# Optimization experiments

Measured on AMD Instinct MI355X. Metric: run time of the kernel, lower is better.

Reference implementation:

```python
import jax, jax.numpy as jnp
import numpy as np

N_NODES = 50000
N_HEDGES = 25000
E_NN = 800000
E_HH = 400000
E_INC = 200000
D = 128


def setup_inputs() -> dict:
    key = jax.random.key(0)
    ks = jax.random.split(key, 24)
    s = 1.0 / np.sqrt(D)
    inp = {
        'node_features': jax.random.normal(ks[0], (N_NODES, D), jnp.float32),
        'hedge_features': jax.random.normal(ks[1], (N_HEDGES, D), jnp.float32),
        'W_node_msg': jax.random.normal(ks[2], (D, D), jnp.float32) * s,
        'b_node_msg': jax.random.normal(ks[3], (D,), jnp.float32) * s,
        'W_hedge_scale': jax.random.normal(ks[4], (D, D), jnp.float32) * s,
        'b_hedge_scale': jax.random.normal(ks[5], (D,), jnp.float32) * s,
        'W_hedge_msg': jax.random.normal(ks[6], (D, D), jnp.float32) * s,
        'b_hedge_msg': jax.random.normal(ks[7], (D,), jnp.float32) * s,
        'W_node_scale': jax.random.normal(ks[8], (D, D), jnp.float32) * s,
        'b_node_scale': jax.random.normal(ks[9], (D,), jnp.float32) * s,
        'node_convolution': jax.random.uniform(ks[10], (E_NN, 1), jnp.float32),
        'hedge2node_convolution': jax.random.uniform(ks[11], (E_INC, 1), jnp.float32),
        'hedge_convolution': jax.random.uniform(ks[12], (E_HH, 1), jnp.float32),
        'node2hedge_convolution': jax.random.uniform(ks[13], (E_INC, 1), jnp.float32),
        'node_senders': jax.random.randint(ks[14], (E_NN,), 0, N_NODES, jnp.int32),
        'node_receivers': jax.random.randint(ks[15], (E_NN,), 0, N_NODES, jnp.int32),
        'hedge2node_senders': jax.random.randint(ks[16], (E_INC,), 0, N_HEDGES, jnp.int32),
        'hedge2node_receivers': jax.random.randint(ks[17], (E_INC,), 0, N_NODES, jnp.int32),
        'hedge_senders': jax.random.randint(ks[18], (E_HH,), 0, N_HEDGES, jnp.int32),
        'hedge_receivers': jax.random.randint(ks[19], (E_HH,), 0, N_HEDGES, jnp.int32),
        'node2hedge_senders': jax.random.randint(ks[20], (E_INC,), 0, N_NODES, jnp.int32),
        'node2hedge_receivers': jax.random.randint(ks[21], (E_INC,), 0, N_HEDGES, jnp.int32),
    }
    return inp


def _lin(x, W, b):
    # eqx.nn.Linear: y = W @ x + b, vmapped over rows -> x @ W.T + b
    return x @ W.T + b


def reference(node_features, hedge_features,
              W_node_msg, b_node_msg, W_hedge_scale, b_hedge_scale,
              W_hedge_msg, b_hedge_msg, W_node_scale, b_node_scale,
              node_convolution, hedge2node_convolution,
              hedge_convolution, node2hedge_convolution,
              node_senders, node_receivers,
              hedge2node_senders, hedge2node_receivers,
              hedge_senders, hedge_receivers,
              node2hedge_senders, node2hedge_receivers):
    n_nodes = node_features.shape[0]
    n_hedges = hedge_features.shape[0]

    # --- NodeConvolution ---
    msgs = _lin(node_features[node_senders], W_node_msg, b_node_msg)  # [E_nn, D]
    gathered_msgs = jax.ops.segment_sum(node_convolution * msgs, node_receivers,
                                        num_segments=n_nodes)
    h_msgs = _lin(hedge_features[hedge2node_senders], W_hedge_scale, b_hedge_scale)
    gathered_scale = jax.ops.segment_sum(hedge2node_convolution * h_msgs,
                                         hedge2node_receivers, num_segments=n_nodes)
    new_node_features = jnp.tanh(gathered_scale * gathered_msgs)

    # --- HedgeConvolution (uses updated node features) ---
    e_msgs = _lin(hedge_features[hedge_senders], W_hedge_msg, b_hedge_msg)  # [E_hh, D]
    gathered_e = jax.ops.segment_sum(hedge_convolution * e_msgs, hedge_receivers,
                                     num_segments=n_hedges)
    n_msgs = _lin(new_node_features[node2hedge_senders], W_node_scale, b_node_scale)
    gathered_n = jax.ops.segment_sum(node2hedge_convolution * n_msgs,
                                     node2hedge_receivers, num_segments=n_hedges)
    new_hedge_features = jnp.tanh(gathered_n * gathered_e)

    return (new_node_features, new_hedge_features)
```

## Files before the change

kernel.cpp:

```cpp
#include <hip/hip_runtime.h>
#include <hip/hip_bf16.h>

#define N_NODES  50000
#define N_HEDGES 25000
#define E_NN     800000
#define E_HH     400000
#define E_INC    200000
#define D        128

__global__ __launch_bounds__(256) void swizzleW(
    const float* __restrict__ w0, const float* __restrict__ w1,
    const float* __restrict__ w2, const float* __restrict__ w3,
    float* __restrict__ out) {
  int id = blockIdx.x * 256 + threadIdx.x;
  int m = id >> 14, r = id & 16383;
  const float* w = (m == 0) ? w0 : (m == 1) ? w1 : (m == 2) ? w2 : w3;
  int c = r >> 7, k = r & 127;
  out[m * 16512 + (c >> 2) * 516 + (k >> 2) * 16 + (c & 3) * 4 + (k & 3)] = w[r];
}

__global__ __launch_bounds__(256) void linear64(
    const float* __restrict__ X, const float* __restrict__ Wz,
    const float* __restrict__ bias, float* __restrict__ Y, int n) {
  __shared__ float Ws[16 * 516];
  __shared__ float Xs[64 * 132];
  int t = threadIdx.x;
  int r0 = blockIdx.x * 64;
  int cb = blockIdx.y * 64;

  const float* wsrc = Wz + blockIdx.y * (16 * 516);
  for (int i = t * 4; i < 16 * 516; i += 1024)
    *(float4*)(Ws + i) = *(const float4*)(wsrc + i);

  for (int q = t; q < 2048; q += 256) {
    int r = q >> 5, k4 = q & 31;
    float4 v = (r0 + r < n) ? *(const float4*)(X + (size_t)(r0 + r) * D + k4 * 4)
                            : make_float4(0.f, 0.f, 0.f, 0.f);
    *(float4*)(&Xs[r * 132 + k4 * 4]) = v;
  }
  __syncthreads();

  int tr = t >> 4, tc = t & 15;
  float acc[4][4] = {};
  const float* xbase = &Xs[tr * 4 * 132];
  const float* wbase = &Ws[tc * 516];

#pragma unroll 8
  for (int k4 = 0; k4 < 32; ++k4) {
    float4 xv[4], wv[4];
#pragma unroll
    for (int i = 0; i < 4; ++i) xv[i] = *(const float4*)(xbase + i * 132 + k4 * 4);
#pragma unroll
    for (int j = 0; j < 4; ++j) wv[j] = *(const float4*)(wbase + k4 * 16 + j * 4);
#pragma unroll
    for (int i = 0; i < 4; ++i)
#pragma unroll
      for (int j = 0; j < 4; ++j)
        acc[i][j] += xv[i].x * wv[j].x + xv[i].y * wv[j].y +
                     xv[i].z * wv[j].z + xv[i].w * wv[j].w;
  }

  int c0 = cb + tc * 4;
  float4 bv = *(const float4*)(bias + c0);
#pragma unroll
  for (int i = 0; i < 4; ++i) {
    int r = r0 + tr * 4 + i;
    if (r < n) {
      float4 o;
      o.x = acc[i][0] + bv.x; o.y = acc[i][1] + bv.y;
      o.z = acc[i][2] + bv.z; o.w = acc[i][3] + bv.w;
      *(float4*)(Y + (size_t)r * D + c0) = o;
    }
  }
}

#define B_NN   3125
#define B_H2N  782
#define B_HH   1563
#define B_N2H  782
#define B_TOT  (B_NN + B_H2N + B_HH + B_N2H)

__global__ __launch_bounds__(256) void hist4(
    const int* __restrict__ rNN, const int* __restrict__ rH2N,
    const int* __restrict__ rHH, const int* __restrict__ rN2H,
    int* __restrict__ cNN, int* __restrict__ cH2N,
    int* __restrict__ cHH, int* __restrict__ cN2H) {
  int b = blockIdx.x;
  const int* rcv; int* cnt; int E, base;
  if (b < B_NN)                { rcv = rNN;  cnt = cNN;  E = E_NN;  base = 0; }
  else if (b < B_NN + B_H2N)   { rcv = rH2N; cnt = cH2N; E = E_INC; base = B_NN; }
  else if (b < B_NN + B_H2N + B_HH) { rcv = rHH; cnt = cHH; E = E_HH; base = B_NN + B_H2N; }
  else                         { rcv = rN2H; cnt = cN2H; E = E_INC; base = B_NN + B_H2N + B_HH; }
  int i = (b - base) * 256 + threadIdx.x;
  if (i < E) atomicAdd(&cnt[rcv[i]], 1);
}

__global__ __launch_bounds__(1024) void exscan4(
    const int* __restrict__ c0, int* __restrict__ o0, int* __restrict__ u0,
    const int* __restrict__ c1, int* __restrict__ o1, int* __restrict__ u1,
    const int* __restrict__ c2, int* __restrict__ o2, int* __restrict__ u2,
    const int* __restrict__ c3, int* __restrict__ o3, int* __restrict__ u3) {
  const int* c; int* offs; int* cur; int n;
  switch (blockIdx.x) {
    case 0:  c = c0; offs = o0; cur = u0; n = N_NODES;  break;
    case 1:  c = c1; offs = o1; cur = u1; n = N_NODES;  break;
    case 2:  c = c2; offs = o2; cur = u2; n = N_HEDGES; break;
    default: c = c3; offs = o3; cur = u3; n = N_HEDGES; break;
  }
  __shared__ int wsum[16];
  __shared__ int carrySh;
  int lane = threadIdx.x & 63, wid = threadIdx.x >> 6;
  if (threadIdx.x == 0) carrySh = 0;
  __syncthreads();
  for (int base = 0; base < n; base += 4096) {
    int i0 = base + threadIdx.x * 4;
    int v[4];
#pragma unroll
    for (int j = 0; j < 4; ++j) { int i = i0 + j; v[j] = (i < n) ? c[i] : 0; }
    int s = v[0] + v[1] + v[2] + v[3];
    int inc = s;
#pragma unroll
    for (int off = 1; off < 64; off <<= 1) {
      int tv = __shfl_up(inc, off, 64);
      if (lane >= off) inc += tv;
    }
    if (lane == 63) wsum[wid] = inc;
    __syncthreads();
    if (threadIdx.x == 0) {
      int run = 0;
      for (int w = 0; w < 16; ++w) { int x = wsum[w]; wsum[w] = run; run += x; }
    }
    __syncthreads();
    int run = carrySh + wsum[wid] + (inc - s);
#pragma unroll
    for (int j = 0; j < 4; ++j) {
      int i = i0 + j;
      if (i < n) { offs[i] = run; cur[i] = run; }
      run += v[j];
    }
    __syncthreads();
    if (threadIdx.x == 1023) carrySh = run;
    __syncthreads();
  }
  if (threadIdx.x == 0) offs[n] = carrySh;
}

__global__ __launch_bounds__(256) void fill4(
    const int* __restrict__ rNN, const int* __restrict__ sNN,
    const float* __restrict__ vNN, int* __restrict__ uNN, int2* __restrict__ pNN,
    const int* __restrict__ rH2N, const int* __restrict__ sH2N,
    const float* __restrict__ vH2N, int* __restrict__ uH2N, int2* __restrict__ pH2N,
    const int* __restrict__ rHH, const int* __restrict__ sHH,
    const float* __restrict__ vHH, int* __restrict__ uHH, int2* __restrict__ pHH,
    const int* __restrict__ rN2H, const int* __restrict__ sN2H,
    const float* __restrict__ vN2H, int* __restrict__ uN2H, int2* __restrict__ pN2H) {
  int b = blockIdx.x;
  const int* rcv; const int* snd; const float* cv; int* cur; int2* pr; int E, base;
  if (b < B_NN)                { rcv = rNN;  snd = sNN;  cv = vNN;  cur = uNN;  pr = pNN;  E = E_NN;  base = 0; }
  else if (b < B_NN + B_H2N)   { rcv = rH2N; snd = sH2N; cv = vH2N; cur = uH2N; pr = pH2N; E = E_INC; base = B_NN; }
  else if (b < B_NN + B_H2N + B_HH) { rcv = rHH; snd = sHH; cv = vHH; cur = uHH; pr = pHH; E = E_HH; base = B_NN + B_H2N; }
  else                         { rcv = rN2H; snd = sN2H; cv = vN2H; cur = uN2H; pr = pN2H; E = E_INC; base = B_NN + B_H2N + B_HH; }
  int i = (b - base) * 256 + threadIdx.x;
  if (i < E) {
    int p = atomicAdd(&cur[rcv[i]], 1);
    pr[p] = make_int2(snd[i], __float_as_int(cv[i]));
  }
}

__global__ __launch_bounds__(256) void gather_combine2(
    const float* __restrict__ Pa, const int2* __restrict__ pairsA,
    const int* __restrict__ offsA,
    const float* __restrict__ Pb, const int2* __restrict__ pairsB,
    const int* __restrict__ offsB,
    float* __restrict__ out, int nrows) {
  int row = (blockIdx.x << 2) | (threadIdx.x >> 6);
  if (row >= nrows) return;
  int lane = threadIdx.x & 63;

  float sax = 0.f, say = 0.f;
  {
    int a0 = offsA[row], a1 = offsA[row + 1];
    int i = a0;
    for (; i + 8 <= a1; i += 8) {
      int2 p[8]; float2 v[8];
#pragma unroll
      for (int j = 0; j < 8; ++j) p[j] = pairsA[i + j];
#pragma unroll
      for (int j = 0; j < 8; ++j)
        v[j] = *(const float2*)(Pa + (size_t)p[j].x * D + lane * 2);
#pragma unroll
      for (int j = 0; j < 8; ++j) {
        float c = __int_as_float(p[j].y);
        sax += c * v[j].x; say += c * v[j].y;
      }
    }
    for (; i + 4 <= a1; i += 4) {
      int2 p[4]; float2 v[4];
#pragma unroll
      for (int j = 0; j < 4; ++j) p[j] = pairsA[i + j];
#pragma unroll
      for (int j = 0; j < 4; ++j)
        v[j] = *(const float2*)(Pa + (size_t)p[j].x * D + lane * 2);
#pragma unroll
      for (int j = 0; j < 4; ++j) {
        float c = __int_as_float(p[j].y);
        sax += c * v[j].x; say += c * v[j].y;
      }
    }
    for (; i < a1; ++i) {
      int2 p = pairsA[i];
      float c = __int_as_float(p.y);
      float2 v = *(const float2*)(Pa + (size_t)p.x * D + lane * 2);
      sax += c * v.x; say += c * v.y;
    }
  }

  float sbx = 0.f, sby = 0.f;
  {
    int b0 = offsB[row], b1 = offsB[row + 1];
    int i = b0;
    for (; i + 4 <= b1; i += 4) {
      int2 p[4]; float2 v[4];
#pragma unroll
      for (int j = 0; j < 4; ++j) p[j] = pairsB[i + j];
#pragma unroll
      for (int j = 0; j < 4; ++j)
        v[j] = *(const float2*)(Pb + (size_t)p[j].x * D + lane * 2);
#pragma unroll
      for (int j = 0; j < 4; ++j) {
        float c = __int_as_float(p[j].y);
        sbx += c * v[j].x; sby += c * v[j].y;
      }
    }
    for (; i < b1; ++i) {
      int2 p = pairsB[i];
      float c = __int_as_float(p.y);
      float2 v = *(const float2*)(Pb + (size_t)p.x * D + lane * 2);
      sbx += c * v.x; sby += c * v.y;
    }
  }

  float2 o;
  o.x = tanhf(sax * sbx);
  o.y = tanhf(say * sby);
  *(float2*)(out + (size_t)row * D + lane * 2) = o;
}

extern "C" void kernel_launch(void* const* d_in, const int* in_sizes, int n_in,
                              void* d_out, int out_size, void* d_ws, size_t ws_size,
                              hipStream_t stream) {
  const float* node_features  = (const float*)d_in[0];
  const float* hedge_features = (const float*)d_in[1];
  const float* W_node_msg     = (const float*)d_in[2];
  const float* b_node_msg     = (const float*)d_in[3];
  const float* W_hedge_scale  = (const float*)d_in[4];
  const float* b_hedge_scale  = (const float*)d_in[5];
  const float* W_hedge_msg    = (const float*)d_in[6];
  const float* b_hedge_msg    = (const float*)d_in[7];
  const float* W_node_scale   = (const float*)d_in[8];
  const float* b_node_scale   = (const float*)d_in[9];
  const float* node_conv      = (const float*)d_in[10];
  const float* h2n_conv       = (const float*)d_in[11];
  const float* hedge_conv     = (const float*)d_in[12];
  const float* n2h_conv       = (const float*)d_in[13];
  const int*   node_snd       = (const int*)d_in[14];
  const int*   node_rcv       = (const int*)d_in[15];
  const int*   h2n_snd        = (const int*)d_in[16];
  const int*   h2n_rcv        = (const int*)d_in[17];
  const int*   hedge_snd      = (const int*)d_in[18];
  const int*   hedge_rcv      = (const int*)d_in[19];
  const int*   n2h_snd        = (const int*)d_in[20];
  const int*   n2h_rcv        = (const int*)d_in[21];

  float* out_node  = (float*)d_out;
  float* out_hedge = (float*)d_out + (size_t)N_NODES * D;

  float* ws = (float*)d_ws;
  float* Wz = ws;
  float* PA = ws + 66048;
  float* PB = PA + (size_t)N_NODES * D;
  int2* pairsNN  = (int2*)(PB + (size_t)N_HEDGES * D);
  int2* pairsH2N = pairsNN + E_NN;
  int2* pairsHH  = pairsH2N + E_INC;
  int2* pairsN2H = pairsHH + E_HH;
  int* cntNN  = (int*)(pairsN2H + E_INC);
  int* cntH2N = cntNN + N_NODES;
  int* cntHH  = cntH2N + N_NODES;
  int* cntN2H = cntHH + N_HEDGES;
  int* curNN  = cntN2H + N_HEDGES;
  int* curH2N = curNN + N_NODES;
  int* curHH  = curH2N + N_NODES;
  int* curN2H = curHH + N_HEDGES;
  int* offsNN  = curN2H + N_HEDGES;
  int* offsH2N = offsNN + N_NODES + 1;
  int* offsHH  = offsH2N + N_NODES + 1;
  int* offsN2H = offsHH + N_HEDGES + 1;

  swizzleW<<<256, 256, 0, stream>>>(W_node_msg, W_hedge_scale, W_hedge_msg,
                                    W_node_scale, Wz);
  hipMemsetAsync(cntNN, 0, (size_t)(2 * (N_NODES + N_HEDGES)) * sizeof(int), stream);

  hist4<<<B_TOT, 256, 0, stream>>>(node_rcv, h2n_rcv, hedge_rcv, n2h_rcv,
                                   cntNN, cntH2N, cntHH, cntN2H);
  exscan4<<<4, 1024, 0, stream>>>(cntNN, offsNN, curNN,
                                  cntH2N, offsH2N, curH2N,
                                  cntHH, offsHH, curHH,
                                  cntN2H, offsN2H, curN2H);
  fill4<<<B_TOT, 256, 0, stream>>>(
      node_rcv, node_snd, node_conv, curNN, pairsNN,
      h2n_rcv, h2n_snd, h2n_conv, curH2N, pairsH2N,
      hedge_rcv, hedge_snd, hedge_conv, curHH, pairsHH,
      n2h_rcv, n2h_snd, n2h_conv, curN2H, pairsN2H);

  linear64<<<dim3(782, 2), 256, 0, stream>>>(node_features, Wz + 0 * 16512,
                                             b_node_msg, PA, N_NODES);
  linear64<<<dim3(391, 2), 256, 0, stream>>>(hedge_features, Wz + 1 * 16512,
                                             b_hedge_scale, PB, N_HEDGES);
  gather_combine2<<<N_NODES / 4, 256, 0, stream>>>(
      PA, pairsNN, offsNN, PB, pairsH2N, offsH2N, out_node, N_NODES);

  linear64<<<dim3(391, 2), 256, 0, stream>>>(hedge_features, Wz + 2 * 16512,
                                             b_hedge_msg, PB, N_HEDGES);
  linear64<<<dim3(782, 2), 256, 0, stream>>>(out_node, Wz + 3 * 16512,
                                             b_node_scale, PA, N_NODES);
  gather_combine2<<<N_HEDGES / 4, 256, 0, stream>>>(
      PB, pairsHH, offsHH, PA, pairsN2H, offsN2H, out_hedge, N_HEDGES);
}
```

Before: 602.4 us.

## Replace serial scan and scatter fill with parallel scan and two-pass bucketed CSR build

The single-block-per-array exclusive scan becomes a three-kernel multi-block scan (block scans, scan of block sums, add-back). The one-pass atomic scatter fill becomes a two-pass bucketed scatter. Pass A groups edges into 64-receiver buckets using shared-memory histograms and per-bucket global atomics. Pass B places each bucket's edges into final CSR positions, so the scattered writes stay local. This targets the serial scan latency and the poorly coalesced random scatter, at the cost of extra kernel launches and an intermediate record buffer that is written and read once.

Result: faster. 548.0 us (-9.0%).

```diff
diff --git a/kernel.cpp b/kernel.cpp
--- a/kernel.cpp
+++ b/kernel.cpp
@@ -95,75 +95,187 @@
   if (i < E) atomicAdd(&cnt[rcv[i]], 1);
 }
 
-__global__ __launch_bounds__(1024) void exscan4(
-    const int* __restrict__ c0, int* __restrict__ o0, int* __restrict__ u0,
-    const int* __restrict__ c1, int* __restrict__ o1, int* __restrict__ u1,
-    const int* __restrict__ c2, int* __restrict__ o2, int* __restrict__ u2,
-    const int* __restrict__ c3, int* __restrict__ o3, int* __restrict__ u3) {
-  const int* c; int* offs; int* cur; int n;
-  switch (blockIdx.x) {
-    case 0:  c = c0; offs = o0; cur = u0; n = N_NODES;  break;
-    case 1:  c = c1; offs = o1; cur = u1; n = N_NODES;  break;
-    case 2:  c = c2; offs = o2; cur = u2; n = N_HEDGES; break;
-    default: c = c3; offs = o3; cur = u3; n = N_HEDGES; break;
-  }
-  __shared__ int wsum[16];
-  __shared__ int carrySh;
-  int lane = threadIdx.x & 63, wid = threadIdx.x >> 6;
-  if (threadIdx.x == 0) carrySh = 0;
-  __syncthreads();
-  for (int base = 0; base < n; base += 4096) {
-    int i0 = base + threadIdx.x * 4;
-    int v[4];
-#pragma unroll
-    for (int j = 0; j < 4; ++j) { int i = i0 + j; v[j] = (i < n) ? c[i] : 0; }
-    int s = v[0] + v[1] + v[2] + v[3];
-    int inc = s;
-#pragma unroll
-    for (int off = 1; off < 64; off <<= 1) {
-      int tv = __shfl_up(inc, off, 64);
-      if (lane >= off) inc += tv;
-    }
-    if (lane == 63) wsum[wid] = inc;
-    __syncthreads();
-    if (threadIdx.x == 0) {
-      int run = 0;
-      for (int w = 0; w < 16; ++w) { int x = wsum[w]; wsum[w] = run; run += x; }
-    }
-    __syncthreads();
-    int run = carrySh + wsum[wid] + (inc - s);
-#pragma unroll
-    for (int j = 0; j < 4; ++j) {
-      int i = i0 + j;
-      if (i < n) { offs[i] = run; cur[i] = run; }
-      run += v[j];
-    }
-    __syncthreads();
-    if (threadIdx.x == 1023) carrySh = run;
-    __syncthreads();
-  }
-  if (threadIdx.x == 0) offs[n] = carrySh;
-}
-
-__global__ __launch_bounds__(256) void fill4(
-    const int* __restrict__ rNN, const int* __restrict__ sNN,
-    const float* __restrict__ vNN, int* __restrict__ uNN, int2* __restrict__ pNN,
-    const int* __restrict__ rH2N, const int* __restrict__ sH2N,
-    const float* __restrict__ vH2N, int* __restrict__ uH2N, int2* __restrict__ pH2N,
-    const int* __restrict__ rHH, const int* __restrict__ sHH,
-    const float* __restrict__ vHH, int* __restrict__ uHH, int2* __restrict__ pHH,
-    const int* __restrict__ rN2H, const int* __restrict__ sN2H,
-    const float* __restrict__ vN2H, int* __restrict__ uN2H, int2* __restrict__ pN2H) {
+#define SB_NN0  0
+#define SB_H2N0 25
+#define SB_HH0  50
+#define SB_N2H0 63
+#define SB_TOT  76
+
+__global__ __launch_bounds__(256) void scan_blk(
+    const int* __restrict__ cNN, const int* __restrict__ cH2N,
+    const int* __restrict__ cHH, const int* __restrict__ cN2H,
+    int* __restrict__ oNN, int* __restrict__ oH2N,
+    int* __restrict__ oHH, int* __restrict__ oN2H,
+    int* __restrict__ bsum) {
   int b = blockIdx.x;
-  const int* rcv; const int* snd; const float* cv; int* cur; int2* pr; int E, base;
-  if (b < B_NN)                { rcv = rNN;  snd = sNN;  cv = vNN;  cur = uNN;  pr = pNN;  E = E_NN;  base = 0; }
-  else if (b < B_NN + B_H2N)   { rcv = rH2N; snd = sH2N; cv = vH2N; cur = uH2N; pr = pH2N; E = E_INC; base = B_NN; }
-  else if (b < B_NN + B_H2N + B_HH) { rcv = rHH; snd = sHH; cv = vHH; cur = uHH; pr = pHH; E = E_HH; base = B_NN + B_H2N; }
-  else                         { rcv = rN2H; snd = sN2H; cv = vN2H; cur = uN2H; pr = pN2H; E = E_INC; base = B_NN + B_H2N + B_HH; }
-  int i = (b - base) * 256 + threadIdx.x;
-  if (i < E) {
-    int p = atomicAdd(&cur[rcv[i]], 1);
-    pr[p] = make_int2(snd[i], __float_as_int(cv[i]));
+  const int* c; int* o; int n; int lb;
+  if (b < SB_H2N0)       { c = cNN;  o = oNN;  n = N_NODES;  lb = b; }
+  else if (b < SB_HH0)   { c = cH2N; o = oH2N; n = N_NODES;  lb = b - SB_H2N0; }
+  else if (b < SB_N2H0)  { c = cHH;  o = oHH;  n = N_HEDGES; lb = b - SB_HH0; }
+  else                   { c = cN2H; o = oN2H; n = N_HEDGES; lb = b - SB_N2H0; }
+  int t = threadIdx.x, lane = t & 63, wid = t >> 6;
+  int i0 = lb * 2048 + t * 8;
+  int v[8]; int s = 0;
+#pragma unroll
+  for (int j = 0; j < 8; ++j) { int i = i0 + j; v[j] = (i < n) ? c[i] : 0; s += v[j]; }
+  int inc = s;
+#pragma unroll
+  for (int off = 1; off < 64; off <<= 1) {
+    int tv = __shfl_up(inc, off, 64);
+    if (lane >= off) inc += tv;
+  }
+  __shared__ int wsum[4];
+  if (lane == 63) wsum[wid] = inc;
+  __syncthreads();
+  if (t == 0) {
+    int run = 0;
+    for (int w = 0; w < 4; ++w) { int x = wsum[w]; wsum[w] = run; run += x; }
+  }
+  __syncthreads();
+  int run = wsum[wid] + (inc - s);
+#pragma unroll
+  for (int j = 0; j < 8; ++j) { int i = i0 + j; if (i < n) o[i] = run; run += v[j]; }
+  if (t == 255) bsum[b] = run;
+}
+
+__global__ void scan_bsum(int* __restrict__ bsum,
+                          int* __restrict__ oNN, int* __restrict__ oH2N,
+                          int* __restrict__ oHH, int* __restrict__ oN2H) {
+  int a = threadIdx.x;
+  if (a >= 4) return;
+  int base = (a == 0) ? SB_NN0 : (a == 1) ? SB_H2N0 : (a == 2) ? SB_HH0 : SB_N2H0;
+  int cnt  = (a < 2) ? 25 : 13;
+  int run = 0;
+  for (int i = 0; i < cnt; ++i) { int x = bsum[base + i]; bsum[base + i] = run; run += x; }
+  int* o = (a == 0) ? oNN : (a == 1) ? oH2N : (a == 2) ? oHH : oN2H;
+  int n = (a < 2) ? N_NODES : N_HEDGES;
+  o[n] = run;
+}
+
+__global__ __launch_bounds__(256) void scan_add(
+    int* __restrict__ oNN, int* __restrict__ oH2N,
+    int* __restrict__ oHH, int* __restrict__ oN2H,
+    int* __restrict__ uNN, int* __restrict__ uH2N,
+    int* __restrict__ uHH, int* __restrict__ uN2H,
+    const int* __restrict__ bsum) {
+  int b = blockIdx.x;
+  int* o; int* u; int n; int lb;
+  if (b < SB_H2N0)       { o = oNN;  u = uNN;  n = N_NODES;  lb = b; }
+  else if (b < SB_HH0)   { o = oH2N; u = uH2N; n = N_NODES;  lb = b - SB_H2N0; }
+  else if (b < SB_N2H0)  { o = oHH;  u = uHH;  n = N_HEDGES; lb = b - SB_HH0; }
+  else                   { o = oN2H; u = uN2H; n = N_HEDGES; lb = b - SB_N2H0; }
+  int add = bsum[b];
+  int i0 = lb * 2048 + threadIdx.x * 8;
+#pragma unroll
+  for (int j = 0; j < 8; ++j) {
+    int i = i0 + j;
+    if (i < n) { int x = o[i] + add; o[i] = x; u[i] = x; }
+  }
+}
+
+#define NB_NN   782
+#define NB_H2N  782
+#define NB_HH   391
+#define NB_N2H  391
+#define NB_TOT  (NB_NN + NB_H2N + NB_HH + NB_N2H)
+#define NB_MAX  782
+
+#define REC_NN  0
+#define REC_H2N 800000
+#define REC_HH  1000000
+#define REC_N2H 1400000
+
+__global__ __launch_bounds__(256) void initb(
+    const int* __restrict__ oNN, const int* __restrict__ oH2N,
+    const int* __restrict__ oHH, const int* __restrict__ oN2H,
+    int* __restrict__ bcur) {
+  int i = blockIdx.x * 256 + threadIdx.x;
+  if (i >= NB_TOT) return;
+  int v;
+  if (i < NB_NN)                        v = oNN[i << 6];
+  else if (i < NB_NN + NB_H2N)          v = oH2N[(i - NB_NN) << 6];
+  else if (i < NB_NN + NB_H2N + NB_HH)  v = oHH[(i - NB_NN - NB_H2N) << 6];
+  else                                  v = oN2H[(i - NB_NN - NB_H2N - NB_HH) << 6];
+  bcur[i] = v;
+}
+
+#define PA_NN0  0
+#define PA_H2N0 391
+#define PA_HH0  489
+#define PA_N2H0 685
+#define PA_TOT  783
+
+__global__ __launch_bounds__(256) void passA(
+    const int* __restrict__ sNN, const int* __restrict__ rNN, const float* __restrict__ vNN,
+    const int* __restrict__ sH2N, const int* __restrict__ rH2N, const float* __restrict__ vH2N,
+    const int* __restrict__ sHH, const int* __restrict__ rHH, const float* __restrict__ vHH,
+    const int* __restrict__ sN2H, const int* __restrict__ rN2H, const float* __restrict__ vN2H,
+    int* __restrict__ bcur, int2* __restrict__ rec_sc, int* __restrict__ rec_r) {
+  __shared__ int hist[NB_MAX];
+  __shared__ int gbase[NB_MAX];
+  __shared__ int lcur[NB_MAX];
+  int b = blockIdx.x;
+  const int* snd; const int* rcv; const float* conv;
+  int E, blkbase, bcoff, recoff, NB;
+  if (b < PA_H2N0)      { snd=sNN;  rcv=rNN;  conv=vNN;  E=E_NN;  blkbase=PA_NN0;  bcoff=0;    recoff=REC_NN;  NB=NB_NN; }
+  else if (b < PA_HH0)  { snd=sH2N; rcv=rH2N; conv=vH2N; E=E_INC; blkbase=PA_H2N0; bcoff=782;  recoff=REC_H2N; NB=NB_H2N; }
+  else if (b < PA_N2H0) { snd=sHH;  rcv=rHH;  conv=vHH;  E=E_HH;  blkbase=PA_HH0;  bcoff=1564; recoff=REC_HH;  NB=NB_HH; }
+  else                  { snd=sN2H; rcv=rN2H; conv=vN2H; E=E_INC; blkbase=PA_N2H0; bcoff=1955; recoff=REC_N2H; NB=NB_N2H; }
+  int t = threadIdx.x;
+  int estart = (b - blkbase) * 2048;
+
+  int rv[8]; int sd[8]; float cv[8]; int bk[8]; bool ok[8];
+#pragma unroll
+  for (int j = 0; j < 8; ++j) {
+    int e = estart + t + j * 256;
+    ok[j] = e < E;
+    int r = ok[j] ? rcv[e] : 0;
+    rv[j] = r;
+    bk[j] = r >> 6;
+    sd[j] = ok[j] ? snd[e] : 0;
+    cv[j] = ok[j] ? conv[e] : 0.f;
+  }
+  for (int i = t; i < NB; i += 256) hist[i] = 0;
+  __syncthreads();
+#pragma unroll
+  for (int j = 0; j < 8; ++j) if (ok[j]) atomicAdd(&hist[bk[j]], 1);
+  __syncthreads();
+  for (int i = t; i < NB; i += 256) {
+    int h = hist[i];
+    gbase[i] = h ? atomicAdd(&bcur[bcoff + i], h) : 0;
+    lcur[i] = 0;
+  }
+  __syncthreads();
+#pragma unroll
+  for (int j = 0; j < 8; ++j) if (ok[j]) {
+    int rk = atomicAdd(&lcur[bk[j]], 1);
+    int g = recoff + gbase[bk[j]] + rk;
+    rec_sc[g] = make_int2(sd[j], __float_as_int(cv[j]));
+    rec_r[g] = rv[j];
+  }
+}
+
+__global__ __launch_bounds__(256) void passB(
+    const int2* __restrict__ rec_sc, const int* __restrict__ rec_r,
+    const int* __restrict__ oNN, const int* __restrict__ oH2N,
+    const int* __restrict__ oHH, const int* __restrict__ oN2H,
+    int* __restrict__ uNN, int* __restrict__ uH2N,
+    int* __restrict__ uHH, int* __restrict__ uN2H,
+    int2* __restrict__ pairs) {
+  int b = blockIdx.x;
+  const int* offs; int* cur; int n, lb, recoff;
+  if (b < NB_NN)                        { offs = oNN;  cur = uNN;  n = N_NODES;  lb = b;                          recoff = REC_NN; }
+  else if (b < NB_NN + NB_H2N)          { offs = oH2N; cur = uH2N; n = N_NODES;  lb = b - NB_NN;                  recoff = REC_H2N; }
+  else if (b < NB_NN + NB_H2N + NB_HH)  { offs = oHH;  cur = uHH;  n = N_HEDGES; lb = b - NB_NN - NB_H2N;         recoff = REC_HH; }
+  else                                  { offs = oN2H; cur = uN2H; n = N_HEDGES; lb = b - NB_NN - NB_H2N - NB_HH; recoff = REC_N2H; }
+  int r0 = lb << 6;
+  int r1 = min(r0 + 64, n);
+  int base = offs[r0], end = offs[r1];
+  for (int i = base + (int)threadIdx.x; i < end; i += 256) {
+    int2 sc = rec_sc[recoff + i];
+    int rvv = rec_r[recoff + i];
+    int p = atomicAdd(&cur[rvv], 1);
+    pairs[recoff + p] = sc;
   }
 }
 
@@ -279,11 +391,10 @@
   float* Wz = ws;
   float* PA = ws + 66048;
   float* PB = PA + (size_t)N_NODES * D;
-  int2* pairsNN  = (int2*)(PB + (size_t)N_HEDGES * D);
-  int2* pairsH2N = pairsNN + E_NN;
-  int2* pairsHH  = pairsH2N + E_INC;
-  int2* pairsN2H = pairsHH + E_HH;
-  int* cntNN  = (int*)(pairsN2H + E_INC);
+  int2* pairs   = (int2*)(PB + (size_t)N_HEDGES * D);
+  int2* rec_sc  = pairs + 1600000;
+  int*  rec_r   = (int*)(rec_sc + 1600000);
+  int* cntNN  = rec_r + 1600000;
   int* cntH2N = cntNN + N_NODES;
   int* cntHH  = cntH2N + N_NODES;
   int* cntN2H = cntHH + N_HEDGES;
@@ -295,6 +406,13 @@
   int* offsH2N = offsNN + N_NODES + 1;
   int* offsHH  = offsH2N + N_NODES + 1;
   int* offsN2H = offsHH + N_HEDGES + 1;
+  int* bsum    = offsN2H + N_HEDGES + 1;
+  int* bcur    = bsum + SB_TOT;
+
+  int2* pairsNN  = pairs;
+  int2* pairsH2N = pairs + REC_H2N;
+  int2* pairsHH  = pairs + REC_HH;
+  int2* pairsN2H = pairs + REC_N2H;
 
   swizzleW<<<256, 256, 0, stream>>>(W_node_msg, W_hedge_scale, W_hedge_msg,
                                     W_node_scale, Wz);
@@ -302,15 +420,22 @@
 
   hist4<<<B_TOT, 256, 0, stream>>>(node_rcv, h2n_rcv, hedge_rcv, n2h_rcv,
                                    cntNN, cntH2N, cntHH, cntN2H);
-  exscan4<<<4, 1024, 0, stream>>>(cntNN, offsNN, curNN,
-                                  cntH2N, offsH2N, curH2N,
-                                  cntHH, offsHH, curHH,
-                                  cntN2H, offsN2H, curN2H);
-  fill4<<<B_TOT, 256, 0, stream>>>(
-      node_rcv, node_snd, node_conv, curNN, pairsNN,
-      h2n_rcv, h2n_snd, h2n_conv, curH2N, pairsH2N,
-      hedge_rcv, hedge_snd, hedge_conv, curHH, pairsHH,
-      n2h_rcv, n2h_snd, n2h_conv, curN2H, pairsN2H);
+  scan_blk<<<SB_TOT, 256, 0, stream>>>(cntNN, cntH2N, cntHH, cntN2H,
+                                       offsNN, offsH2N, offsHH, offsN2H, bsum);
+  scan_bsum<<<1, 64, 0, stream>>>(bsum, offsNN, offsH2N, offsHH, offsN2H);
+  scan_add<<<SB_TOT, 256, 0, stream>>>(offsNN, offsH2N, offsHH, offsN2H,
+                                       curNN, curH2N, curHH, curN2H, bsum);
+  initb<<<(NB_TOT + 255) / 256, 256, 0, stream>>>(offsNN, offsH2N, offsHH, offsN2H, bcur);
+  passA<<<PA_TOT, 256, 0, stream>>>(
+      node_snd, node_rcv, node_conv,
+      h2n_snd, h2n_rcv, h2n_conv,
+      hedge_snd, hedge_rcv, hedge_conv,
+      n2h_snd, n2h_rcv, n2h_conv,
+      bcur, rec_sc, rec_r);
+  passB<<<NB_TOT, 256, 0, stream>>>(
+      rec_sc, rec_r,
+      offsNN, offsH2N, offsHH, offsN2H,
+      curNN, curH2N, curHH, curN2H, pairs);
 
   linear64<<<dim3(782, 2), 256, 0, stream>>>(node_features, Wz + 0 * 16512,
                                              b_node_msg, PA, N_NODES);
```
